# Kernel tuning notes

Measured on AMD Instinct MI355X. Metric: run time of the kernel, lower is better.

## Reference

```python
import jax, jax.numpy as jnp
import numpy as np
from jax import lax

B, C, H, W = 4, 32, 512, 512
DN = ('NCHW', 'OIHW', 'NCHW')

# cv2 correlation kernels (filter2D/Sobel/Scharr do correlation, not convolution)
SOBEL_X = np.array([[-1, 0, 1], [-2, 0, 2], [-1, 0, 1]], np.float32)
SOBEL_Y = SOBEL_X.T
SCHARR_X = np.array([[-3, 0, 3], [-10, 0, 10], [-3, 0, 3]], np.float32)
SCHARR_Y = SCHARR_X.T
LAPLACE3 = np.array([[2, 0, 2], [0, -8, 0], [2, 0, 2]], np.float32)  # cv2.Laplacian ksize=3
ROBERTS_X = np.array([[-1, 0], [0, 1]], np.float32)
ROBERTS_Y = np.array([[0, -1], [1, 0]], np.float32)
PREWITT_X = np.array([[1, 1, 1], [0, 0, 0], [-1, -1, -1]], np.float32)
PREWITT_Y = np.array([[-1, 0, 1], [-1, 0, 1], [-1, 0, 1]], np.float32)


def _corr(x, k, pad_hw):
    # per-channel 2D correlation with cv2 BORDER_REFLECT_101 padding
    b, c, h, w = x.shape
    xp = jnp.pad(x, ((0, 0), (0, 0), pad_hw[0], pad_hw[1]), mode='reflect')
    kj = jnp.asarray(k)[None, None]  # (1,1,kh,kw)
    y = lax.conv_general_dilated(xp.reshape(b * c, 1, xp.shape[2], xp.shape[3]),
                                 kj, (1, 1), 'VALID', dimension_numbers=DN)
    return y.reshape(b, c, h, w)


def _norm(x):
    # Norm(): per-sample zero-mean/unit-std over all of (C,H,W)
    m = jnp.mean(x, axis=(1, 2, 3), keepdims=True)
    s = jnp.std(x, axis=(1, 2, 3), keepdims=True)
    return (x - m) / s


def get_operator(x):
    p3 = ((1, 1), (1, 1))          # 3x3 kernel, anchor (1,1)
    p2 = ((1, 0), (1, 0))          # 2x2 kernel, cv2 default anchor (1,1)
    b1 = _norm(0.5 * _corr(x, SOBEL_X, p3) + 0.5 * _corr(x, SOBEL_Y, p3))
    b2 = _norm(0.5 * _corr(x, SCHARR_X, p3) + 0.5 * _corr(x, SCHARR_Y, p3))
    b3 = _norm(_corr(x, LAPLACE3, p3))
    b4 = _norm(0.5 * _corr(x, ROBERTS_X, p2) + 0.5 * _corr(x, ROBERTS_Y, p2))
    b5 = _norm(0.5 * _corr(x, PREWITT_X, p3) + 0.5 * _corr(x, PREWITT_Y, p3))
    return jnp.concatenate([b1, b2, b3, b4, b5], axis=1)


def conv3x3(x, w, b):
    y = lax.conv_general_dilated(x, w, (1, 1), [(1, 1), (1, 1)], dimension_numbers=DN)
    return y + b[None, :, None, None]


def maxpool2(x):
    b, c, h, w = x.shape
    return x.reshape(b, c, h // 2, 2, w // 2, 2).max(axis=(3, 5))


def deconv2x2(x, w, b):
    # ConvTranspose2d(k=2, s=2): each pixel expands to a 2x2 block; w is (Cin,Cout,2,2)
    bb, ci, h, wd = x.shape
    y = jnp.einsum('bihw,iopq->bohpwq', x, w).reshape(bb, w.shape[1], 2 * h, 2 * wd)
    return y + b[None, :, None, None]


def setup_inputs():
    key = jax.random.key(0)
    ks = jax.random.split(key, 24)
    def uni(k, shape, fan_in):
        bd = 1.0 / np.sqrt(fan_in)
        return jax.random.uniform(k, shape, jnp.float32, -bd, bd)
    d = {'x': jax.random.normal(ks[0], (B, C, H, W), jnp.float32)}
    d['conv1_w'] = uni(ks[1], (C, 5 * C, 3, 3), 5 * C * 9)
    d['conv1_b'] = uni(ks[2], (C,), 5 * C * 9)
    for i, name in enumerate(['conv2', 'conv3', 'conv4', 'conv5', 'conv6', 'conv7']):
        d[name + '_w'] = uni(ks[3 + 2 * i], (C, C, 3, 3), C * 9)
        d[name + '_b'] = uni(ks[4 + 2 * i], (C,), C * 9)
    for i, name in enumerate(['deconv1', 'deconv2', 'deconv3']):
        d[name + '_w'] = uni(ks[15 + 2 * i], (C, C, 2, 2), C * 4)
        d[name + '_b'] = uni(ks[16 + 2 * i], (C,), C * 4)
    return d


def reference(x, conv1_w, conv1_b, conv2_w, conv2_b, conv3_w, conv3_b, conv4_w, conv4_b,
              conv5_w, conv5_b, conv6_w, conv6_b, conv7_w, conv7_b,
              deconv1_w, deconv1_b, deconv2_w, deconv2_b, deconv3_w, deconv3_b):
    orig = x
    y = get_operator(x)                      # (B, 5C, H, W)
    y = conv3x3(y, conv1_w, conv1_b)
    y = maxpool2(y)
    y = conv3x3(y, conv2_w, conv2_b)
    y = maxpool2(y)
    y = conv3x3(y, conv3_w, conv3_b)
    y = maxpool2(y)
    y = conv3x3(y, conv4_w, conv4_b)
    y = deconv2x2(y, deconv1_w, deconv1_b)   # sizes divide evenly -> no interpolate
    y = conv3x3(y, conv5_w, conv5_b)
    y = deconv2x2(y, deconv2_w, deconv2_b)
    y = conv3x3(y, conv6_w, conv6_b)
    y = deconv2x2(y, deconv3_w, deconv3_b)
    y = conv3x3(y, conv7_w, conv7_b)
    return orig * y
```

## Files before the change

### kernel.cpp

```cpp
#include <hip/hip_runtime.h>
#include <hip/hip_bf16.h>
#include <cstddef>


typedef unsigned short u16;
typedef unsigned int uint;
typedef __attribute__((ext_vector_type(8))) short short8v;
typedef __attribute__((ext_vector_type(4))) float float4v;

constexpr int Bn = 4, Cn = 32, Hn = 512, Wn = 512;
constexpr int PLANE = Hn * Wn;

__device__ __forceinline__ float b2f(u16 u) {
  union { uint i; float f; } c; c.i = ((uint)u) << 16; return c.f;
}
__device__ __forceinline__ u16 f2b(float f) {
  union { float f; uint i; } c; c.f = f;
  uint r = c.i + 0x7FFFu + ((c.i >> 16) & 1u);
  return (u16)(r >> 16);
}

static __device__ __forceinline__ int reflect_idx(int i, int n) {
  return i < 0 ? -i : (i >= n ? 2 * n - 2 - i : i);
}

#define BRANCH_VALS(n00, n01, n02, n10, n11, n12, n20, n21, n22, v1, v2, v3, v4, v5)        \
  do {                                                                                      \
    v1 = -(n00 + n01 + n10) + (n12 + n21 + n22);                                            \
    v2 = -3.f * n00 - 5.f * n01 - 5.f * n10 + 5.f * n12 + 5.f * n21 + 3.f * n22;            \
    v3 = 2.f * (n00 + n02 + n20 + n22) - 8.f * n11;                                         \
    v4 = 0.5f * (-n00 - n01 + n10 + n11);                                                   \
    v5 = 0.5f * n01 + n02 - 0.5f * n10 + 0.5f * n12 - n20 - 0.5f * n21;                     \
  } while (0)

__device__ const float Sdev[5][9] = {
    {-1.f, -1.f, 0.f, -1.f, 0.f, 1.f, 0.f, 1.f, 1.f},
    {-3.f, -5.f, 0.f, -5.f, 0.f, 5.f, 0.f, 5.f, 3.f},
    {2.f, 0.f, 2.f, 0.f, -8.f, 0.f, 2.f, 0.f, 2.f},
    {-0.5f, -0.5f, 0.f, 0.5f, 0.5f, 0.f, 0.f, 0.f, 0.f},
    {0.f, 0.5f, 1.f, -0.5f, 0.f, 0.5f, -1.f, -0.5f, 0.f}};

__global__ void __launch_bounds__(128) k_opstats(const float* __restrict__ x,
                                                 float* __restrict__ partS,
                                                 float* __restrict__ partQ) {
  int bid = blockIdx.x;
  int b = bid >> 11;
  int local = bid & 2047;
  int c = local >> 6;
  int chunk = local & 63;
  int t = threadIdx.x;
  int w0 = t * 4;
  const float* xp = x + (size_t)(b * Cn + c) * PLANE;
  int h0 = chunk * 8;

  int ci[6];
#pragma unroll
  for (int j = 0; j < 6; j++) ci[j] = reflect_idx(w0 - 1 + j, Wn);

  float ap[6], ac[6], an[6];
  {
    const float* rp = xp + reflect_idx(h0 - 1, Hn) * Wn;
#pragma unroll
    for (int j = 0; j < 6; j++) ap[j] = rp[ci[j]];
  }
  {
    const float* rp = xp + h0 * Wn;
#pragma unroll
    for (int j = 0; j < 6; j++) ac[j] = rp[ci[j]];
  }

  float s[5] = {0, 0, 0, 0, 0}, q[5] = {0, 0, 0, 0, 0};
#pragma unroll
  for (int r = 0; r < 8; ++r) {
    int h = h0 + r;
    const float* rp = xp + reflect_idx(h + 1, Hn) * Wn;
#pragma unroll
    for (int j = 0; j < 6; j++) an[j] = rp[ci[j]];
#pragma unroll
    for (int k = 0; k < 4; ++k) {
      float v1, v2, v3, v4, v5;
      BRANCH_VALS(ap[k], ap[k + 1], ap[k + 2], ac[k], ac[k + 1], ac[k + 2],
                  an[k], an[k + 1], an[k + 2], v1, v2, v3, v4, v5);
      s[0] += v1; q[0] += v1 * v1;
      s[1] += v2; q[1] += v2 * v2;
      s[2] += v3; q[2] += v3 * v3;
      s[3] += v4; q[3] += v4 * v4;
      s[4] += v5; q[4] += v5 * v5;
    }
#pragma unroll
    for (int j = 0; j < 6; j++) { ap[j] = ac[j]; ac[j] = an[j]; }
  }

#pragma unroll
  for (int i = 0; i < 5; i++) {
    float ss = s[i], qq = q[i];
#pragma unroll
    for (int off = 32; off > 0; off >>= 1) {
      ss += __shfl_down(ss, off);
      qq += __shfl_down(qq, off);
    }
    if ((t & 63) == 0) {
      int wv = t >> 6;
      int g = b * 5 + i;
      int idx = (c * 64 + chunk) * 2 + wv;
      partS[(size_t)g * 4096 + idx] = ss;
      partQ[(size_t)g * 4096 + idx] = qq;
    }
  }
}

__global__ void __launch_bounds__(256) k_stats(const float* __restrict__ partS,
                                               const float* __restrict__ partQ,
                                               float* __restrict__ stats) {
  __shared__ float red[256];
  int g = blockIdx.x;
  int t = threadIdx.x;
  float ss = 0.f, qq = 0.f;
  const float* ps = partS + (size_t)g * 4096;
  const float* pq = partQ + (size_t)g * 4096;
  for (int i = t; i < 4096; i += 256) {
    ss += ps[i];
    qq += pq[i];
  }
  red[t] = ss;
  __syncthreads();
  for (int o = 128; o > 0; o >>= 1) {
    if (t < o) red[t] += red[t + o];
    __syncthreads();
  }
  float S = red[0];
  __syncthreads();
  red[t] = qq;
  __syncthreads();
  for (int o = 128; o > 0; o >>= 1) {
    if (t < o) red[t] += red[t + o];
    __syncthreads();
  }
  if (t == 0) {
    const float N = 8388608.0f;
    float mean = S / N;
    float var = red[0] / N - mean * mean;
    stats[g * 2] = mean;
    stats[g * 2 + 1] = 1.0f / sqrtf(var);
  }
}

__global__ void __launch_bounds__(256) k_prep_shared(
    const float* w2, const float* w3, const float* w4, const float* w5,
    const float* w6, const float* w7, const float* dw1, const float* dw2,
    const float* dw3, u16* A2, u16* A3, u16* A4, u16* A5, u16* A6, u16* A7,
    u16* Ad1, u16* Ad2, u16* Ad3) {
  int id = blockIdx.x * 256 + threadIdx.x;
  if (id < 55296) {
    int s = id / 9216, r = id % 9216;
    int tap = r / 1024, oc = (r >> 5) & 31, ic = r & 31;
    const float* w = s == 0 ? w2 : s == 1 ? w3 : s == 2 ? w4 : s == 3 ? w5 : s == 4 ? w6 : w7;
    u16* A = s == 0 ? A2 : s == 1 ? A3 : s == 2 ? A4 : s == 3 ? A5 : s == 4 ? A6 : A7;
    A[r] = f2b(w[(oc * 32 + ic) * 9 + tap]);
  } else if (id < 67584) {
    int r = id - 55296;
    int s = r / 4096, e = r % 4096;
    int par = e >> 10, oc = (e >> 5) & 31, ic = e & 31;
    const float* w = s == 0 ? dw1 : s == 1 ? dw2 : dw3;
    u16* A = s == 0 ? Ad1 : s == 1 ? Ad2 : Ad3;
    A[e] = f2b(w[(ic * 32 + oc) * 4 + par]);
  }
}

__global__ void __launch_bounds__(256) k_prep_conv1(const float* __restrict__ w1,
                                                    const float* __restrict__ b1,
                                                    const float* __restrict__ stats,
                                                    u16* __restrict__ A5c,
                                                    float* __restrict__ bias1all) {
  int e = blockIdx.x * 256 + threadIdx.x;
  if (e < 102400) {
    int b = e / 25600, r = e % 25600;
    int tap = r >> 10, oc = (r >> 5) & 31, ic = r & 31;
    int u = tap / 5, v = tap % 5;
    float acc = 0.f;
#pragma unroll
    for (int br = 0; br < 5; ++br) {
      float is = stats[(b * 5 + br) * 2 + 1];
      const float* wp = w1 + ((size_t)oc * 160 + br * 32 + ic) * 9;
      float sub = 0.f;
#pragma unroll
      for (int a = 0; a < 3; ++a) {
        int s = u - a;
        if (s < 0 || s > 2) continue;
#pragma unroll
        for (int bb = 0; bb < 3; ++bb) {
          int tt = v - bb;
          if (tt < 0 || tt > 2) continue;
          sub += wp[a * 3 + bb] * Sdev[br][s * 3 + tt];
        }
      }
      acc += is * sub;
    }
    A5c[e] = f2b(acc);
  } else if (e < 102528) {
    int t2 = e - 102400;
    int b = t2 >> 5, oc = t2 & 31;
    float s = 0.f;
    for (int ch = 0; ch < 160; ++ch) {
      int br = ch >> 5;
      float mi = stats[(b * 5 + br) * 2] * stats[(b * 5 + br) * 2 + 1];
      const float* wp = w1 + (size_t)(oc * 160 + ch) * 9;
      float ws = 0.f;
#pragma unroll
      for (int tap = 0; tap < 9; ++tap) ws += wp[tap];
      s += ws * mi;
    }
    bias1all[b * 32 + oc] = b1[oc] - s;
  }
}

__global__ void __launch_bounds__(256) k_conv5x5(const float* __restrict__ x,
                                                 const u16* __restrict__ A5c,
                                                 const float* __restrict__ biasAll,
                                                 u16* __restrict__ outb) {
  __shared__ __align__(16) u16 bs[400 * 32];
  int t = threadIdx.x;
  int l = t & 63, wv = t >> 6, ln = l & 15, q = l >> 4;
  int b = blockIdx.z;
  int h0 = blockIdx.y * 16, w0 = blockIdx.x * 16;

  {
    int cp = t & 15;
    int px0 = t >> 4;
    int py = 0, pxx = px0;
    const float* xp0 = x + ((size_t)b * 32 + 2 * cp) * PLANE;
    const float* xp1 = xp0 + PLANE;
#pragma unroll
    for (int i = 0; i < 25; ++i) {
      int gh = reflect_idx(h0 - 2 + py, Hn);
      int gw = reflect_idx(w0 - 2 + pxx, Wn);
      float v0 = xp0[gh * Wn + gw];
      float v1 = xp1[gh * Wn + gw];
      int px = py * 20 + pxx;
      uint pk = (uint)f2b(v0) | ((uint)f2b(v1) << 16);
      *(uint*)((char*)bs + px * 64 + ((((cp >> 2) ^ (px & 3)) << 4)) + (cp & 3) * 4) = pk;
      pxx += 16;
      if (pxx >= 20) { pxx -= 20; py += 1; }
    }
  }
  __syncthreads();

  float4v acc[4][2];
#pragma unroll
  for (int i = 0; i < 4; ++i) {
    acc[i][0] = (float4v){0.f, 0.f, 0.f, 0.f};
    acc[i][1] = (float4v){0.f, 0.f, 0.f, 0.f};
  }

  const u16* Ab = A5c + (size_t)b * 25600;
#pragma unroll
  for (int ty = 0; ty < 5; ++ty) {
#pragma unroll
    for (int tx = 0; tx < 5; ++tx) {
      int tap = ty * 5 + tx;
      short8v af0 = *(const short8v*)&Ab[((size_t)tap * 32 + ln) * 32 + q * 8];
      short8v af1 = *(const short8v*)&Ab[((size_t)tap * 32 + 16 + ln) * 32 + q * 8];
#pragma unroll
      for (int r4 = 0; r4 < 4; ++r4) {
        int px = (wv * 4 + r4 + ty) * 20 + ln + tx;
        short8v bf = *(const short8v*)((const char*)bs + px * 64 + ((q ^ (px & 3)) << 4));
        acc[r4][0] = __builtin_amdgcn_mfma_f32_16x16x32_bf16(af0, bf, acc[r4][0], 0, 0, 0);
        acc[r4][1] = __builtin_amdgcn_mfma_f32_16x16x32_bf16(af1, bf, acc[r4][1], 0, 0, 0);
      }
    }
  }

  const float* bias = biasAll + b * 32;
#pragma unroll
  for (int rp = 0; rp < 2; ++rp) {
#pragma unroll
    for (int g = 0; g < 2; ++g) {
      float m0 = fmaxf(acc[2 * rp][g][0], acc[2 * rp + 1][g][0]);
      float m1 = fmaxf(acc[2 * rp][g][1], acc[2 * rp + 1][g][1]);
      float m2 = fmaxf(acc[2 * rp][g][2], acc[2 * rp + 1][g][2]);
      float m3 = fmaxf(acc[2 * rp][g][3], acc[2 * rp + 1][g][3]);
      m0 = fmaxf(m0, __shfl_xor(m0, 1));
      m1 = fmaxf(m1, __shfl_xor(m1, 1));
      m2 = fmaxf(m2, __shfl_xor(m2, 1));
      m3 = fmaxf(m3, __shfl_xor(m3, 1));
      if (!(l & 1)) {
        int ph = (h0 >> 1) + wv * 2 + rp;
        int pw = (w0 >> 1) + (ln >> 1);
        uint2 pk;
        pk.x = (uint)f2b(m0 + bias[g * 16 + q * 4 + 0]) |
               ((uint)f2b(m1 + bias[g * 16 + q * 4 + 1]) << 16);
        pk.y = (uint)f2b(m2 + bias[g * 16 + q * 4 + 2]) |
               ((uint)f2b(m3 + bias[g * 16 + q * 4 + 3]) << 16);
        *(uint2*)&outb[(((size_t)b * 256 + ph) * 256 + pw) * 32 + g * 16 + q * 4] = pk;
      }
    }
  }
}

__global__ void __launch_bounds__(256) k_border(const float* __restrict__ x,
                                                const float* __restrict__ w1,
                                                const float* __restrict__ b1,
                                                const float* __restrict__ stats,
                                                u16* __restrict__ p1) {
  int t = threadIdx.x;
  int lane = t & 63, quad = t >> 6;
  int b = blockIdx.y;
  int p = blockIdx.x * 64 + lane;
  if (p >= 4080) return;
  int cell = p >> 2, k = p & 3;
  int ph, pw;
  if (cell < 256) { ph = 0; pw = cell; }
  else if (cell < 512) { ph = 255; pw = cell - 256; }
  else if (cell < 766) { ph = 1 + (cell - 512); pw = 0; }
  else { ph = 1 + (cell - 766); pw = 255; }
  int h = 2 * ph + (k >> 1), w = 2 * pw + (k & 1);

  float mean[5], istd[5];
#pragma unroll
  for (int br = 0; br < 5; ++br) {
    mean[br] = stats[(b * 5 + br) * 2];
    istd[br] = stats[(b * 5 + br) * 2 + 1];
  }

  float acc[8];
#pragma unroll
  for (int i = 0; i < 8; ++i) acc[i] = 0.f;

  for (int c = 0; c < 32; ++c) {
    const float* xp = x + (size_t)(b * 32 + c) * PLANE;
    float xw[5][5];
#pragma unroll
    for (int dy = 0; dy < 5; ++dy) {
      int gh = reflect_idx(h - 2 + dy, Hn);
#pragma unroll
      for (int dx = 0; dx < 5; ++dx) {
        int gw = reflect_idx(w - 2 + dx, Wn);
        xw[dy][dx] = xp[gh * Wn + gw];
      }
    }
    float Bnv[5][9];
#pragma unroll
    for (int ty = 0; ty < 3; ++ty) {
#pragma unroll
      for (int tx = 0; tx < 3; ++tx) {
        int hh = h + ty - 1, ww = w + tx - 1;
        bool valid = (hh >= 0 && hh < Hn && ww >= 0 && ww < Wn);
        float v1, v2, v3, v4, v5;
        BRANCH_VALS(xw[ty][tx], xw[ty][tx + 1], xw[ty][tx + 2],
                    xw[ty + 1][tx], xw[ty + 1][tx + 1], xw[ty + 1][tx + 2],
                    xw[ty + 2][tx], xw[ty + 2][tx + 1], xw[ty + 2][tx + 2],
                    v1, v2, v3, v4, v5);
        int tap = ty * 3 + tx;
        Bnv[0][tap] = valid ? (v1 - mean[0]) * istd[0] : 0.f;
        Bnv[1][tap] = valid ? (v2 - mean[1]) * istd[1] : 0.f;
        Bnv[2][tap] = valid ? (v3 - mean[2]) * istd[2] : 0.f;
        Bnv[3][tap] = valid ? (v4 - mean[3]) * istd[3] : 0.f;
        Bnv[4][tap] = valid ? (v5 - mean[4]) * istd[4] : 0.f;
      }
    }
#pragma unroll
    for (int br = 0; br < 5; ++br) {
#pragma unroll
      for (int oc8 = 0; oc8 < 8; ++oc8) {
        int oc = quad * 8 + oc8;
        const float* wp = w1 + ((size_t)oc * 160 + br * 32 + c) * 9;
        float a0 = acc[oc8];
#pragma unroll
        for (int tap = 0; tap < 9; ++tap) a0 = fmaf(wp[tap], Bnv[br][tap], a0);
        acc[oc8] = a0;
      }
    }
  }

  u16 r[8];
#pragma unroll
  for (int oc8 = 0; oc8 < 8; ++oc8) {
    float m = acc[oc8] + b1[quad * 8 + oc8];
    m = fmaxf(m, __shfl_xor(m, 1));
    m = fmaxf(m, __shfl_xor(m, 2));
    r[oc8] = f2b(m);
  }
  if (k == 0)
    *(uint4*)&p1[(((size_t)b * 256 + ph) * 256 + pw) * 32 + quad * 8] = *(uint4*)r;
}

template <int CIN, int MODE>
__global__ void __launch_bounds__(256) k_conv_mfma(const u16* __restrict__ in,
                                                   const u16* __restrict__ Aw,
                                                   const float* __restrict__ bias,
                                                   u16* __restrict__ outb,
                                                   float* __restrict__ outf,
                                                   const float* __restrict__ xorig,
                                                   int H, int W) {
  constexpr int ICC = CIN / 32;
  __shared__ __align__(16) char smem[20736];
  u16* bs = (u16*)smem;
  int t = threadIdx.x;
  int l = t & 63, wv = t >> 6;
  int ln = l & 15, q = l >> 4;
  int bz = blockIdx.z;
  int h0 = blockIdx.y * 16, w0 = blockIdx.x * 16;

  float4v acc[4][2];
#pragma unroll
  for (int i = 0; i < 4; ++i) {
    acc[i][0] = (float4v){0.f, 0.f, 0.f, 0.f};
    acc[i][1] = (float4v){0.f, 0.f, 0.f, 0.f};
  }

  for (int icc = 0; icc < ICC; ++icc) {
    for (int u = t; u < 1296; u += 256) {
      int px = u >> 2, sq = u & 3;
      int ry = px / 18, rx = px - ry * 18;
      int gh = h0 - 1 + ry, gw = w0 - 1 + rx;
      uint4 v = {0, 0, 0, 0};
      if (gh >= 0 && gh < H && gw >= 0 && gw < W)
        v = *(const uint4*)&in[(((size_t)bz * H + gh) * W + gw) * CIN + icc * 32 + sq * 8];
      *(uint4*)((char*)bs + px * 64 + ((sq ^ (px & 3)) << 4)) = v;
    }
    short8v af[9][2];
#pragma unroll
    for (int tp = 0; tp < 9; ++tp) {
      af[tp][0] = *(const short8v*)&Aw[((size_t)(icc * 9 + tp) * 32 + ln) * 32 + q * 8];
      af[tp][1] = *(const short8v*)&Aw[((size_t)(icc * 9 + tp) * 32 + 16 + ln) * 32 + q * 8];
    }
    __syncthreads();
#pragma unroll
    for (int r4 = 0; r4 < 4; ++r4) {
      int r = wv * 4 + r4;
#pragma unroll
      for (int dy = 0; dy < 3; ++dy) {
#pragma unroll
        for (int dx = 0; dx < 3; ++dx) {
          int px = (r + dy) * 18 + ln + dx;
          short8v bf = *(const short8v*)((const char*)bs + px * 64 + ((q ^ (px & 3)) << 4));
          acc[r4][0] = __builtin_amdgcn_mfma_f32_16x16x32_bf16(af[dy * 3 + dx][0], bf, acc[r4][0], 0, 0, 0);
          acc[r4][1] = __builtin_amdgcn_mfma_f32_16x16x32_bf16(af[dy * 3 + dx][1], bf, acc[r4][1], 0, 0, 0);
        }
      }
    }
    if (ICC > 1) __syncthreads();
  }

  if (MODE == 0) {
#pragma unroll
    for (int r4 = 0; r4 < 4; ++r4) {
      int h = h0 + wv * 4 + r4;
      int wpix = w0 + ln;
#pragma unroll
      for (int g = 0; g < 2; ++g) {
        float v0 = acc[r4][g][0] + bias[g * 16 + q * 4 + 0];
        float v1 = acc[r4][g][1] + bias[g * 16 + q * 4 + 1];
        float v2 = acc[r4][g][2] + bias[g * 16 + q * 4 + 2];
        float v3 = acc[r4][g][3] + bias[g * 16 + q * 4 + 3];
        uint2 pk;
        pk.x = (uint)f2b(v0) | ((uint)f2b(v1) << 16);
        pk.y = (uint)f2b(v2) | ((uint)f2b(v3) << 16);
        *(uint2*)&outb[(((size_t)bz * H + h) * W + wpix) * 32 + g * 16 + q * 4] = pk;
      }
    }
  } else if (MODE == 2) {
    int Hp = H >> 1, Wp = W >> 1;
#pragma unroll
    for (int rp = 0; rp < 2; ++rp) {
#pragma unroll
      for (int g = 0; g < 2; ++g) {
        float m0 = fmaxf(acc[2 * rp][g][0], acc[2 * rp + 1][g][0]);
        float m1 = fmaxf(acc[2 * rp][g][1], acc[2 * rp + 1][g][1]);
        float m2 = fmaxf(acc[2 * rp][g][2], acc[2 * rp + 1][g][2]);
        float m3 = fmaxf(acc[2 * rp][g][3], acc[2 * rp + 1][g][3]);
        m0 = fmaxf(m0, __shfl_xor(m0, 1));
        m1 = fmaxf(m1, __shfl_xor(m1, 1));
        m2 = fmaxf(m2, __shfl_xor(m2, 1));
        m3 = fmaxf(m3, __shfl_xor(m3, 1));
        if (!(l & 1)) {
          int ph = (h0 >> 1) + wv * 2 + rp;
          int pw = (w0 >> 1) + (ln >> 1);
          uint2 pk;
          pk.x = (uint)f2b(m0 + bias[g * 16 + q * 4 + 0]) |
                 ((uint)f2b(m1 + bias[g * 16 + q * 4 + 1]) << 16);
          pk.y = (uint)f2b(m2 + bias[g * 16 + q * 4 + 2]) |
                 ((uint)f2b(m3 + bias[g * 16 + q * 4 + 3]) << 16);
          *(uint2*)&outb[(((size_t)bz * Hp + ph) * Wp + pw) * 32 + g * 16 + q * 4] = pk;
        }
      }
    }
  } else {
    float* os = (float*)smem;
#pragma unroll
    for (int g = 0; g < 2; ++g) {
      __syncthreads();
#pragma unroll
      for (int r4 = 0; r4 < 4; ++r4) {
        int hl = wv * 4 + r4;
#pragma unroll
        for (int i = 0; i < 4; ++i) {
          int ocl = q * 4 + i;
          os[(ocl * 16 + hl) * 20 + ln] = acc[r4][g][i] + bias[g * 16 + ocl];
        }
      }
      __syncthreads();
#pragma unroll
      for (int j = 0; j < 4; ++j) {
        int u = t + j * 256;
        int wq = u & 3, hh = (u >> 2) & 15, ocl = u >> 6;
        float4v v = *(const float4v*)&os[(ocl * 16 + hh) * 20 + wq * 4];
        size_t gidx = (((size_t)bz * 32 + g * 16 + ocl) * H + h0 + hh) * W + w0 + wq * 4;
        float4v xo = *(const float4v*)&xorig[gidx];
        v[0] *= xo[0]; v[1] *= xo[1]; v[2] *= xo[2]; v[3] *= xo[3];
        *(float4v*)&outf[gidx] = v;
      }
    }
  }
}

__global__ void __launch_bounds__(256) k_deconv_mfma(const u16* __restrict__ in,
                                                     const u16* __restrict__ Aw,
                                                     const float* __restrict__ bias,
                                                     u16* __restrict__ out,
                                                     int Hi, int Wi) {
  int t = threadIdx.x;
  int l = t & 63, wv = t >> 6, ln = l & 15, q = l >> 4;
  int z = blockIdx.z, b = z >> 2, par = z & 3, p = par >> 1, qpar = par & 1;
  int h0 = blockIdx.y * 16, w0 = blockIdx.x * 16;
  int Ho = Hi * 2, Wo = Wi * 2;
  short8v af0 = *(const short8v*)&Aw[((size_t)par * 32 + ln) * 32 + q * 8];
  short8v af1 = *(const short8v*)&Aw[((size_t)par * 32 + 16 + ln) * 32 + q * 8];
#pragma unroll
  for (int r4 = 0; r4 < 4; ++r4) {
    int h = h0 + wv * 4 + r4;
    short8v bf = *(const short8v*)&in[(((size_t)b * Hi + h) * Wi + w0 + ln) * 32 + q * 8];
    float4v a0 = (float4v){0.f, 0.f, 0.f, 0.f};
    float4v a1 = (float4v){0.f, 0.f, 0.f, 0.f};
    a0 = __builtin_amdgcn_mfma_f32_16x16x32_bf16(af0, bf, a0, 0, 0, 0);
    a1 = __builtin_amdgcn_mfma_f32_16x16x32_bf16(af1, bf, a1, 0, 0, 0);
    int oh = 2 * h + p, ow = 2 * (w0 + ln) + qpar;
    size_t ob = (((size_t)b * Ho + oh) * Wo + ow) * 32;
    uint2 pk;
    pk.x = (uint)f2b(a0[0] + bias[q * 4 + 0]) | ((uint)f2b(a0[1] + bias[q * 4 + 1]) << 16);
    pk.y = (uint)f2b(a0[2] + bias[q * 4 + 2]) | ((uint)f2b(a0[3] + bias[q * 4 + 3]) << 16);
    *(uint2*)&out[ob + q * 4] = pk;
    pk.x = (uint)f2b(a1[0] + bias[16 + q * 4 + 0]) | ((uint)f2b(a1[1] + bias[16 + q * 4 + 1]) << 16);
    pk.y = (uint)f2b(a1[2] + bias[16 + q * 4 + 2]) | ((uint)f2b(a1[3] + bias[16 + q * 4 + 3]) << 16);
    *(uint2*)&out[ob + 16 + q * 4] = pk;
  }
}

extern "C" void kernel_launch(void* const* d_in, const int* in_sizes, int n_in,
                              void* d_out, int out_size, void* d_ws, size_t ws_size,
                              hipStream_t stream) {
  const float* x   = (const float*)d_in[0];
  const float* w1  = (const float*)d_in[1];
  const float* b1  = (const float*)d_in[2];
  const float* w2  = (const float*)d_in[3];
  const float* b2  = (const float*)d_in[4];
  const float* w3  = (const float*)d_in[5];
  const float* b3  = (const float*)d_in[6];
  const float* w4  = (const float*)d_in[7];
  const float* b4  = (const float*)d_in[8];
  const float* w5  = (const float*)d_in[9];
  const float* b5  = (const float*)d_in[10];
  const float* w6  = (const float*)d_in[11];
  const float* b6  = (const float*)d_in[12];
  const float* w7  = (const float*)d_in[13];
  const float* b7  = (const float*)d_in[14];
  const float* dw1 = (const float*)d_in[15];
  const float* db1 = (const float*)d_in[16];
  const float* dw2 = (const float*)d_in[17];
  const float* db2 = (const float*)d_in[18];
  const float* dw3 = (const float*)d_in[19];
  const float* db3 = (const float*)d_in[20];
  float* out = (float*)d_out;
  char* wsb = (char*)d_ws;

  u16* p1  = (u16*)(wsb + 0);
  u16* p2  = (u16*)(wsb + 16777216ull);
  u16* p3  = (u16*)(wsb + 20971520ull);
  u16* t4  = (u16*)(wsb + 22020096ull);
  u16* dc1 = (u16*)(wsb + 23068672ull);
  u16* t5  = (u16*)(wsb + 27262976ull);
  u16* dc2 = (u16*)(wsb + 31457280ull);
  u16* t6  = (u16*)(wsb + 48234496ull);
  u16* dc3 = (u16*)(wsb + 65011712ull);
  u16* A5c = (u16*)(wsb + 132120576ull);
  u16* A2  = (u16*)(wsb + 132325376ull);
  u16* A3  = (u16*)(wsb + 132343808ull);
  u16* A4  = (u16*)(wsb + 132362240ull);
  u16* A5  = (u16*)(wsb + 132380672ull);
  u16* A6  = (u16*)(wsb + 132399104ull);
  u16* A7  = (u16*)(wsb + 132417536ull);
  u16* Ad1 = (u16*)(wsb + 132435968ull);
  u16* Ad2 = (u16*)(wsb + 132444160ull);
  u16* Ad3 = (u16*)(wsb + 132452352ull);
  float* bias1all = (float*)(wsb + 132460544ull);
  float* partS    = (float*)(wsb + 132461056ull);
  float* partQ    = (float*)(wsb + 132788736ull);
  float* stats    = (float*)(wsb + 133116416ull);

  k_prep_shared<<<264, 256, 0, stream>>>(w2, w3, w4, w5, w6, w7, dw1, dw2, dw3,
                                         A2, A3, A4, A5, A6, A7, Ad1, Ad2, Ad3);
  k_opstats<<<8192, 128, 0, stream>>>(x, partS, partQ);
  k_stats<<<20, 256, 0, stream>>>(partS, partQ, stats);
  k_prep_conv1<<<401, 256, 0, stream>>>(w1, b1, stats, A5c, bias1all);

  k_conv5x5<<<dim3(32, 32, 4), 256, 0, stream>>>(x, A5c, bias1all, p1);
  k_border<<<dim3(64, 4), 256, 0, stream>>>(x, w1, b1, stats, p1);

  k_conv_mfma<32, 2><<<dim3(16, 16, 4), 256, 0, stream>>>(p1, A2, b2, p2, nullptr, nullptr, 256, 256);
  k_conv_mfma<32, 2><<<dim3(8, 8, 4), 256, 0, stream>>>(p2, A3, b3, p3, nullptr, nullptr, 128, 128);
  k_conv_mfma<32, 0><<<dim3(4, 4, 4), 256, 0, stream>>>(p3, A4, b4, t4, nullptr, nullptr, 64, 64);
  k_deconv_mfma<<<dim3(4, 4, 16), 256, 0, stream>>>(t4, Ad1, db1, dc1, 64, 64);
  k_conv_mfma<32, 0><<<dim3(8, 8, 4), 256, 0, stream>>>(dc1, A5, b5, t5, nullptr, nullptr, 128, 128);
  k_deconv_mfma<<<dim3(8, 8, 16), 256, 0, stream>>>(t5, Ad2, db2, dc2, 128, 128);
  k_conv_mfma<32, 0><<<dim3(16, 16, 4), 256, 0, stream>>>(dc2, A6, b6, t6, nullptr, nullptr, 256, 256);
  k_deconv_mfma<<<dim3(16, 16, 16), 256, 0, stream>>>(t6, Ad3, db3, dc3, 256, 256);
  k_conv_mfma<32, 1><<<dim3(32, 32, 4), 256, 0, stream>>>(dc3, A7, b7, nullptr, out, x, 512, 512);
}
```

Measured before the change: 847.4 us.

## Replace scalar border conv1 kernel with MFMA edge-tile kernel

The scalar per-pixel border kernel is replaced by an MFMA-based kernel that handles the full 16x16 edge tiles. It stages x into LDS, computes the normalized operator branches with zero padding for out-of-image taps, and runs a bf16 MFMA 3x3 conv per branch with istd-prescaled weights prepared in k_prep_conv1. The interior 5x5 kernel now skips edge tiles. This removes the slow FMA loop that reread global x, but edge tiles now carry extra LDS passes and more weight prep.

```diff
diff --git a/kernel.cpp b/kernel.cpp
--- a/kernel.cpp
+++ b/kernel.cpp
@@ -171,7 +171,8 @@
                                                     const float* __restrict__ b1,
                                                     const float* __restrict__ stats,
                                                     u16* __restrict__ A5c,
-                                                    float* __restrict__ bias1all) {
+                                                    float* __restrict__ bias1all,
+                                                    u16* __restrict__ A1n) {
   int e = blockIdx.x * 256 + threadIdx.x;
   if (e < 102400) {
     int b = e / 25600, r = e % 25600;
@@ -211,6 +212,12 @@
       s += ws * mi;
     }
     bias1all[b * 32 + oc] = b1[oc] - s;
+  } else if (e < 102528 + 184320) {
+    int e2 = e - 102528;
+    int b = e2 / 46080, r = e2 % 46080;
+    int br = r / 9216, r2 = r % 9216;
+    int tap = r2 / 1024, oc = (r2 >> 5) & 31, ic = r2 & 31;
+    A1n[e2] = f2b(w1[((size_t)oc * 160 + br * 32 + ic) * 9 + tap] * stats[(b * 5 + br) * 2 + 1]);
   }
 }
 
@@ -218,6 +225,7 @@
                                                  const u16* __restrict__ A5c,
                                                  const float* __restrict__ biasAll,
                                                  u16* __restrict__ outb) {
+  if (blockIdx.x == 0 || blockIdx.x == 31 || blockIdx.y == 0 || blockIdx.y == 31) return;
   __shared__ __align__(16) u16 bs[400 * 32];
   int t = threadIdx.x;
   int l = t & 63, wv = t >> 6, ln = l & 15, q = l >> 4;
@@ -297,91 +305,134 @@
   }
 }
 
-__global__ void __launch_bounds__(256) k_border(const float* __restrict__ x,
-                                                const float* __restrict__ w1,
-                                                const float* __restrict__ b1,
-                                                const float* __restrict__ stats,
-                                                u16* __restrict__ p1) {
+__global__ void __launch_bounds__(256) k_conv1_edge(const float* __restrict__ x,
+                                                    const u16* __restrict__ A1n,
+                                                    const float* __restrict__ b1,
+                                                    const float* __restrict__ stats,
+                                                    u16* __restrict__ outb) {
+  __shared__ __align__(16) u16 xs[400 * 32];
+  __shared__ __align__(16) u16 bn[324 * 32];
   int t = threadIdx.x;
-  int lane = t & 63, quad = t >> 6;
+  int l = t & 63, wv = t >> 6, ln = l & 15, q = l >> 4;
   int b = blockIdx.y;
-  int p = blockIdx.x * 64 + lane;
-  if (p >= 4080) return;
-  int cell = p >> 2, k = p & 3;
-  int ph, pw;
-  if (cell < 256) { ph = 0; pw = cell; }
-  else if (cell < 512) { ph = 255; pw = cell - 256; }
-  else if (cell < 766) { ph = 1 + (cell - 512); pw = 0; }
-  else { ph = 1 + (cell - 766); pw = 255; }
-  int h = 2 * ph + (k >> 1), w = 2 * pw + (k & 1);
-
-  float mean[5], istd[5];
-#pragma unroll
+  int bid = blockIdx.x;
+  int th, tw;
+  if (bid < 32) { th = 0; tw = bid; }
+  else if (bid < 64) { th = 31; tw = bid - 32; }
+  else if (bid < 94) { th = 1 + (bid - 64); tw = 0; }
+  else { th = 1 + (bid - 94); tw = 31; }
+  int h0 = th * 16, w0 = tw * 16;
+
+  {
+    int cp = t & 15;
+    int px0 = t >> 4;
+    int py = 0, pxx = px0;
+    const float* xp0 = x + ((size_t)b * 32 + 2 * cp) * PLANE;
+    const float* xp1 = xp0 + PLANE;
+#pragma unroll
+    for (int i = 0; i < 25; ++i) {
+      int gh = reflect_idx(h0 - 2 + py, Hn);
+      int gw = reflect_idx(w0 - 2 + pxx, Wn);
+      float v0 = xp0[gh * Wn + gw];
+      float v1 = xp1[gh * Wn + gw];
+      int px = py * 20 + pxx;
+      uint pk = (uint)f2b(v0) | ((uint)f2b(v1) << 16);
+      *(uint*)((char*)xs + px * 64 + ((((cp >> 2) ^ (px & 3)) << 4)) + (cp & 3) * 4) = pk;
+      pxx += 16;
+      if (pxx >= 20) { pxx -= 20; py += 1; }
+    }
+  }
+  __syncthreads();
+
+  float4v acc[4][2];
+#pragma unroll
+  for (int i = 0; i < 4; ++i) {
+    acc[i][0] = (float4v){0.f, 0.f, 0.f, 0.f};
+    acc[i][1] = (float4v){0.f, 0.f, 0.f, 0.f};
+  }
+
   for (int br = 0; br < 5; ++br) {
-    mean[br] = stats[(b * 5 + br) * 2];
-    istd[br] = stats[(b * 5 + br) * 2 + 1];
-  }
-
-  float acc[8];
-#pragma unroll
-  for (int i = 0; i < 8; ++i) acc[i] = 0.f;
-
-  for (int c = 0; c < 32; ++c) {
-    const float* xp = x + (size_t)(b * 32 + c) * PLANE;
-    float xw[5][5];
-#pragma unroll
-    for (int dy = 0; dy < 5; ++dy) {
-      int gh = reflect_idx(h - 2 + dy, Hn);
-#pragma unroll
-      for (int dx = 0; dx < 5; ++dx) {
-        int gw = reflect_idx(w - 2 + dx, Wn);
-        xw[dy][dx] = xp[gh * Wn + gw];
-      }
-    }
-    float Bnv[5][9];
-#pragma unroll
-    for (int ty = 0; ty < 3; ++ty) {
-#pragma unroll
-      for (int tx = 0; tx < 3; ++tx) {
-        int hh = h + ty - 1, ww = w + tx - 1;
-        bool valid = (hh >= 0 && hh < Hn && ww >= 0 && ww < Wn);
-        float v1, v2, v3, v4, v5;
-        BRANCH_VALS(xw[ty][tx], xw[ty][tx + 1], xw[ty][tx + 2],
-                    xw[ty + 1][tx], xw[ty + 1][tx + 1], xw[ty + 1][tx + 2],
-                    xw[ty + 2][tx], xw[ty + 2][tx + 1], xw[ty + 2][tx + 2],
-                    v1, v2, v3, v4, v5);
-        int tap = ty * 3 + tx;
-        Bnv[0][tap] = valid ? (v1 - mean[0]) * istd[0] : 0.f;
-        Bnv[1][tap] = valid ? (v2 - mean[1]) * istd[1] : 0.f;
-        Bnv[2][tap] = valid ? (v3 - mean[2]) * istd[2] : 0.f;
-        Bnv[3][tap] = valid ? (v4 - mean[3]) * istd[3] : 0.f;
-        Bnv[4][tap] = valid ? (v5 - mean[4]) * istd[4] : 0.f;
-      }
-    }
-#pragma unroll
-    for (int br = 0; br < 5; ++br) {
-#pragma unroll
-      for (int oc8 = 0; oc8 < 8; ++oc8) {
-        int oc = quad * 8 + oc8;
-        const float* wp = w1 + ((size_t)oc * 160 + br * 32 + c) * 9;
-        float a0 = acc[oc8];
-#pragma unroll
-        for (int tap = 0; tap < 9; ++tap) a0 = fmaf(wp[tap], Bnv[br][tap], a0);
-        acc[oc8] = a0;
-      }
-    }
-  }
-
-  u16 r[8];
-#pragma unroll
-  for (int oc8 = 0; oc8 < 8; ++oc8) {
-    float m = acc[oc8] + b1[quad * 8 + oc8];
-    m = fmaxf(m, __shfl_xor(m, 1));
-    m = fmaxf(m, __shfl_xor(m, 2));
-    r[oc8] = f2b(m);
-  }
-  if (k == 0)
-    *(uint4*)&p1[(((size_t)b * 256 + ph) * 256 + pw) * 32 + quad * 8] = *(uint4*)r;
+    float mean = stats[(b * 5 + br) * 2];
+    for (int u = t; u < 10368; u += 256) {
+      int ic = u & 31, px = u >> 5;
+      int r = px / 18, c = px - r * 18;
+      float n00, n01, n02, n10, n11, n12, n20, n21, n22;
+      {
+        int p0 = r * 20 + c, p1 = p0 + 1, p2 = p0 + 2;
+        int p3 = p0 + 20, p4 = p3 + 1, p5 = p3 + 2;
+        int p6 = p3 + 20, p7 = p6 + 1, p8 = p6 + 2;
+        int hi = (ic >> 3), lo = (ic & 7) * 2;
+        n00 = b2f(*(const u16*)((const char*)xs + p0 * 64 + ((hi ^ (p0 & 3)) << 4) + lo));
+        n01 = b2f(*(const u16*)((const char*)xs + p1 * 64 + ((hi ^ (p1 & 3)) << 4) + lo));
+        n02 = b2f(*(const u16*)((const char*)xs + p2 * 64 + ((hi ^ (p2 & 3)) << 4) + lo));
+        n10 = b2f(*(const u16*)((const char*)xs + p3 * 64 + ((hi ^ (p3 & 3)) << 4) + lo));
+        n11 = b2f(*(const u16*)((const char*)xs + p4 * 64 + ((hi ^ (p4 & 3)) << 4) + lo));
+        n12 = b2f(*(const u16*)((const char*)xs + p5 * 64 + ((hi ^ (p5 & 3)) << 4) + lo));
+        n20 = b2f(*(const u16*)((const char*)xs + p6 * 64 + ((hi ^ (p6 & 3)) << 4) + lo));
+        n21 = b2f(*(const u16*)((const char*)xs + p7 * 64 + ((hi ^ (p7 & 3)) << 4) + lo));
+        n22 = b2f(*(const u16*)((const char*)xs + p8 * 64 + ((hi ^ (p8 & 3)) << 4) + lo));
+      }
+      float v;
+      if (br == 0) v = -(n00 + n01 + n10) + (n12 + n21 + n22);
+      else if (br == 1) v = -3.f * n00 - 5.f * n01 - 5.f * n10 + 5.f * n12 + 5.f * n21 + 3.f * n22;
+      else if (br == 2) v = 2.f * (n00 + n02 + n20 + n22) - 8.f * n11;
+      else if (br == 3) v = 0.5f * (-n00 - n01 + n10 + n11);
+      else v = 0.5f * n01 + n02 - 0.5f * n10 + 0.5f * n12 - n20 - 0.5f * n21;
+      int gh = h0 - 1 + r, gw = w0 - 1 + c;
+      bool valid = (gh >= 0 && gh < Hn && gw >= 0 && gw < Wn);
+      float outv = valid ? (v - mean) : 0.f;
+      *(u16*)((char*)bn + px * 64 + (((ic >> 3) ^ (px & 3)) << 4) + (ic & 7) * 2) = f2b(outv);
+    }
+    __syncthreads();
+
+    const u16* Ab = A1n + ((size_t)b * 5 + br) * 9216;
+    short8v af[9][2];
+#pragma unroll
+    for (int tp = 0; tp < 9; ++tp) {
+      af[tp][0] = *(const short8v*)&Ab[((size_t)tp * 32 + ln) * 32 + q * 8];
+      af[tp][1] = *(const short8v*)&Ab[((size_t)tp * 32 + 16 + ln) * 32 + q * 8];
+    }
+#pragma unroll
+    for (int r4 = 0; r4 < 4; ++r4) {
+      int rr = wv * 4 + r4;
+#pragma unroll
+      for (int dy = 0; dy < 3; ++dy) {
+#pragma unroll
+        for (int dx = 0; dx < 3; ++dx) {
+          int px = (rr + dy) * 18 + ln + dx;
+          short8v bf = *(const short8v*)((const char*)bn + px * 64 + ((q ^ (px & 3)) << 4));
+          acc[r4][0] = __builtin_amdgcn_mfma_f32_16x16x32_bf16(af[dy * 3 + dx][0], bf, acc[r4][0], 0, 0, 0);
+          acc[r4][1] = __builtin_amdgcn_mfma_f32_16x16x32_bf16(af[dy * 3 + dx][1], bf, acc[r4][1], 0, 0, 0);
+        }
+      }
+    }
+    __syncthreads();
+  }
+
+#pragma unroll
+  for (int rp = 0; rp < 2; ++rp) {
+#pragma unroll
+    for (int g = 0; g < 2; ++g) {
+      float m0 = fmaxf(acc[2 * rp][g][0], acc[2 * rp + 1][g][0]);
+      float m1 = fmaxf(acc[2 * rp][g][1], acc[2 * rp + 1][g][1]);
+      float m2 = fmaxf(acc[2 * rp][g][2], acc[2 * rp + 1][g][2]);
+      float m3 = fmaxf(acc[2 * rp][g][3], acc[2 * rp + 1][g][3]);
+      m0 = fmaxf(m0, __shfl_xor(m0, 1));
+      m1 = fmaxf(m1, __shfl_xor(m1, 1));
+      m2 = fmaxf(m2, __shfl_xor(m2, 1));
+      m3 = fmaxf(m3, __shfl_xor(m3, 1));
+      if (!(l & 1)) {
+        int ph = (h0 >> 1) + wv * 2 + rp;
+        int pw = (w0 >> 1) + (ln >> 1);
+        uint2 pk;
+        pk.x = (uint)f2b(m0 + b1[g * 16 + q * 4 + 0]) |
+               ((uint)f2b(m1 + b1[g * 16 + q * 4 + 1]) << 16);
+        pk.y = (uint)f2b(m2 + b1[g * 16 + q * 4 + 2]) |
+               ((uint)f2b(m3 + b1[g * 16 + q * 4 + 3]) << 16);
+        *(uint2*)&outb[(((size_t)b * 256 + ph) * 256 + pw) * 32 + g * 16 + q * 4] = pk;
+      }
+    }
+  }
 }
 
 template <int CIN, int MODE>
@@ -596,15 +647,16 @@
   float* partS    = (float*)(wsb + 132461056ull);
   float* partQ    = (float*)(wsb + 132788736ull);
   float* stats    = (float*)(wsb + 133116416ull);
+  u16* A1n        = (u16*)(wsb + 133116576ull);
 
   k_prep_shared<<<264, 256, 0, stream>>>(w2, w3, w4, w5, w6, w7, dw1, dw2, dw3,
                                          A2, A3, A4, A5, A6, A7, Ad1, Ad2, Ad3);
   k_opstats<<<8192, 128, 0, stream>>>(x, partS, partQ);
   k_stats<<<20, 256, 0, stream>>>(partS, partQ, stats);
-  k_prep_conv1<<<401, 256, 0, stream>>>(w1, b1, stats, A5c, bias1all);
+  k_prep_conv1<<<1121, 256, 0, stream>>>(w1, b1, stats, A5c, bias1all, A1n);
 
   k_conv5x5<<<dim3(32, 32, 4), 256, 0, stream>>>(x, A5c, bias1all, p1);
-  k_border<<<dim3(64, 4), 256, 0, stream>>>(x, w1, b1, stats, p1);
+  k_conv1_edge<<<dim3(124, 4), 256, 0, stream>>>(x, A1n, b1, stats, p1);
 
   k_conv_mfma<32, 2><<<dim3(16, 16, 4), 256, 0, stream>>>(p1, A2, b2, p2, nullptr, nullptr, 256, 256);
   k_conv_mfma<32, 2><<<dim3(8, 8, 4), 256, 0, stream>>>(p2, A3, b3, p3, nullptr, nullptr, 128, 128);
```

After: 748.0 us. 11.7% less time.
